# Optimization experiments

Hardware: AMD Instinct MI355X
Metric: run time of the kernel (lower is better)

The kernel has to match this reference:

```python
import jax, jax.numpy as jnp
import numpy as np

M, K, N, G = 64, 4096, 11008, 128  # tokens, infeatures, outfeatures, group_size
NUM_GROUPS = K // G  # 32


def _fp8_round_trip(w):
    # Simulate FP8 E4M3 storage of the quantized weight codes.
    return w.astype(jnp.float8_e4m3fn).astype(jnp.float32)


def setup_inputs() -> dict:
    key = jax.random.key(0)
    k1, k2, k3, k4 = jax.random.split(key, 4)
    x = jax.random.normal(k1, (M, K), dtype=jnp.float32)
    # FP8-representable weight codes (post round-trip, stored as f32 values)
    weight = _fp8_round_trip(jax.random.normal(k2, (N, K), dtype=jnp.float32) * 2.0)
    # Per-(out_feature, group) dequant scales, strictly positive
    weight_scale = jax.random.uniform(k3, (N, NUM_GROUPS), dtype=jnp.float32,
                                      minval=0.005, maxval=0.02)
    bias = jax.random.normal(k4, (N,), dtype=jnp.float32)
    return {"x": x, "weight": weight, "weight_scale": weight_scale, "bias": bias}


def reference(x, weight, weight_scale, bias):
    # Dequantize: each group of `G` consecutive in-features of an output row
    # shares one scale -> w_deq[o, i] = weight[o, i] * scale[o, i // G]
    n, k = weight.shape
    g = k // weight_scale.shape[1]
    w_deq = (weight.reshape(n, -1, g) * weight_scale[:, :, None]).reshape(n, k)
    # Fused dequant-matmul: out[m, o] = sum_i x[m, i] * w_deq[o, i] + bias[o]
    out = jnp.einsum("mk,nk->mn", x, w_deq) + bias
    return out
```

## Files before the change

kernel.cpp:

```cpp
#include <hip/hip_runtime.h>


#define Md 64
#define Kd 4096
#define Nd 11008
#define NGROUPS 32
#define BN 64
#define KSPLIT 16
#define KCHUNK (Kd / KSPLIT)
#define NSTEP (KCHUNK / 32)
#define NGRP (KCHUNK / 128)
#define KGS 64

typedef __attribute__((ext_vector_type(8))) __bf16 bf16x8;
typedef __attribute__((ext_vector_type(4))) float f32x4;

__global__ __launch_bounds__(256, 4)
void qlinear_pass1(const float* __restrict__ x,
                   const float* __restrict__ w,
                   const float* __restrict__ scale,
                   float* __restrict__ ws)
{
    const int tid  = threadIdx.x;
    const int wv   = tid >> 6;
    const int lane = tid & 63;
    const int quad = lane >> 4;
    const int ln   = lane & 15;

    const int n0 = blockIdx.x * BN;
    const int ky = blockIdx.y;
    const int k0 = ky * KCHUNK;

    __shared__ __bf16 lds_x[(KCHUNK / 8) * 64 * 8];

    {
        const int m = tid >> 2;
        const int q = tid & 3;
        const float* xp = x + (size_t)m * Kd + k0;
        #pragma unroll
        for (int j = 0; j < 4; ++j) {
            const int c = q * 16 + j * 64;
            float4 a = *(const float4*)(xp + c);
            float4 b = *(const float4*)(xp + c + 4);
            float4 e = *(const float4*)(xp + c + 8);
            float4 d = *(const float4*)(xp + c + 12);
            bf16x8 v0 = {(__bf16)a.x, (__bf16)a.y, (__bf16)a.z, (__bf16)a.w,
                         (__bf16)b.x, (__bf16)b.y, (__bf16)b.z, (__bf16)b.w};
            bf16x8 v1 = {(__bf16)e.x, (__bf16)e.y, (__bf16)e.z, (__bf16)e.w,
                         (__bf16)d.x, (__bf16)d.y, (__bf16)d.z, (__bf16)d.w};
            const int kg = c >> 3;
            *(bf16x8*)&lds_x[(size_t)(kg * KGS + m) * 8]       = v0;
            *(bf16x8*)&lds_x[(size_t)((kg + 1) * KGS + m) * 8] = v1;
        }
    }
    __syncthreads();

    const int nrow = n0 + wv * 16 + ln;
    const float* wp = w + (size_t)nrow * Kd + k0 + quad * 8;

    const float2 sc2 = *(const float2*)(scale + (size_t)nrow * NGROUPS
                                        + ky * NGRP);
    const float sc[2] = {sc2.x, sc2.y};

    f32x4 acc[4];
    #pragma unroll
    for (int t = 0; t < 4; ++t) acc[t] = (f32x4){0.f, 0.f, 0.f, 0.f};

    float4 wb[3][2];
    wb[0][0] = *(const float4*)(wp + 0);
    wb[0][1] = *(const float4*)(wp + 4);
    wb[1][0] = *(const float4*)(wp + 32);
    wb[1][1] = *(const float4*)(wp + 36);

    #pragma unroll
    for (int g = 0; g < NGRP; ++g) {
        f32x4 pg[4];
        #pragma unroll
        for (int t = 0; t < 4; ++t) pg[t] = (f32x4){0.f, 0.f, 0.f, 0.f};

        #pragma unroll
        for (int ks = 0; ks < 4; ++ks) {
            const int step = g * 4 + ks;
            if (step + 2 < NSTEP) {
                const int s = step + 2;
                wb[s % 3][0] = *(const float4*)(wp + s * 32);
                wb[s % 3][1] = *(const float4*)(wp + s * 32 + 4);
            }
            float4 wa = wb[step % 3][0], wbv = wb[step % 3][1];
            bf16x8 wf = {(__bf16)wa.x,  (__bf16)wa.y,  (__bf16)wa.z,  (__bf16)wa.w,
                         (__bf16)wbv.x, (__bf16)wbv.y, (__bf16)wbv.z, (__bf16)wbv.w};
            #pragma unroll
            for (int t = 0; t < 4; ++t) {
                bf16x8 xf = *(const bf16x8*)
                    &lds_x[(size_t)((step * 4 + quad) * KGS + t * 16 + ln) * 8];
                pg[t] = __builtin_amdgcn_mfma_f32_16x16x32_bf16(xf, wf, pg[t],
                                                                0, 0, 0);
            }
        }

        const float s = sc[g];
        #pragma unroll
        for (int t = 0; t < 4; ++t)
            #pragma unroll
            for (int r = 0; r < 4; ++r)
                acc[t][r] += s * pg[t][r];
    }

    float* op = ws + ((size_t)ky * Md) * Nd + n0 + wv * 16 + ln;
    #pragma unroll
    for (int t = 0; t < 4; ++t)
        #pragma unroll
        for (int r = 0; r < 4; ++r)
            op[(size_t)(t * 16 + quad * 4 + r) * Nd] = acc[t][r];
}

__global__ __launch_bounds__(256)
void qlinear_reduce(const float* __restrict__ ws,
                    const float* __restrict__ bias,
                    float* __restrict__ out)
{
    const int idx4 = blockIdx.x * 256 + threadIdx.x;
    if (idx4 >= Md * Nd / 4) return;
    const int n4 = idx4 % (Nd / 4);
    float4 v = *(const float4*)(bias + n4 * 4);
    #pragma unroll
    for (int ky = 0; ky < KSPLIT; ++ky) {
        float4 p = *(const float4*)(ws + (size_t)ky * Md * Nd + (size_t)idx4 * 4);
        v.x += p.x; v.y += p.y; v.z += p.z; v.w += p.w;
    }
    *(float4*)(out + (size_t)idx4 * 4) = v;
}

extern "C" void kernel_launch(void* const* d_in, const int* in_sizes, int n_in,
                              void* d_out, int out_size, void* d_ws, size_t ws_size,
                              hipStream_t stream) {
    const float* x     = (const float*)d_in[0];
    const float* w     = (const float*)d_in[1];
    const float* scale = (const float*)d_in[2];
    const float* bias  = (const float*)d_in[3];
    float* out = (float*)d_out;
    float* ws  = (float*)d_ws;

    dim3 grid1(Nd / BN, KSPLIT);
    qlinear_pass1<<<grid1, 256, 0, stream>>>(x, w, scale, ws);

    const int total4 = Md * Nd / 4;
    qlinear_reduce<<<(total4 + 255) / 256, 256, 0, stream>>>(ws, bias, out);
}
```

Baseline: 278.5 us.

## Pre-convert x to bf16 in a separate kernel and drop LDS staging

Adds a pre-pass kernel that converts x to bf16 once, in the MFMA-friendly interleaved layout, and stores it in the workspace. The main kernel then reads x fragments straight from global memory (L2-resident) with double buffering, removing the per-block LDS fill and __syncthreads. It also issues all weight loads for the chunk up front and folds the group scale into the weight before the bf16 conversion, so the separate per-group partial accumulators go away. The cost is an extra kernel launch, 16 more float4 registers per thread, and a slight change in rounding because the scale is applied before bf16 truncation.

After: 287.8 us. 1.03x slower.

```diff
diff --git a/kernel.cpp b/kernel.cpp
--- a/kernel.cpp
+++ b/kernel.cpp
@@ -7,16 +7,29 @@
 #define NGROUPS 32
 #define BN 64
 #define KSPLIT 16
-#define KCHUNK (Kd / KSPLIT)
-#define NSTEP (KCHUNK / 32)
-#define NGRP (KCHUNK / 128)
-#define KGS 64
+#define KCHUNK 256
+#define NSTEP 8
+#define WS_PART_BYTES ((size_t)KSPLIT * Md * Nd * 4)
 
 typedef __attribute__((ext_vector_type(8))) __bf16 bf16x8;
 typedef __attribute__((ext_vector_type(4))) float f32x4;
 
+__global__ __launch_bounds__(256)
+void xcvt_kernel(const float* __restrict__ x, __bf16* __restrict__ xbf)
+{
+    const int tid = blockIdx.x * 256 + threadIdx.x;
+    const int m   = tid >> 9;
+    const int kgg = tid & 511;
+    const float* xp = x + (size_t)m * Kd + kgg * 8;
+    float4 a = *(const float4*)xp;
+    float4 b = *(const float4*)(xp + 4);
+    bf16x8 v = {(__bf16)a.x, (__bf16)a.y, (__bf16)a.z, (__bf16)a.w,
+                (__bf16)b.x, (__bf16)b.y, (__bf16)b.z, (__bf16)b.w};
+    *(bf16x8*)(xbf + ((size_t)kgg * 64 + m) * 8) = v;
+}
+
 __global__ __launch_bounds__(256, 4)
-void qlinear_pass1(const float* __restrict__ x,
+void qlinear_pass1(const __bf16* __restrict__ xbf,
                    const float* __restrict__ w,
                    const float* __restrict__ scale,
                    float* __restrict__ ws)
@@ -29,81 +42,52 @@
 
     const int n0 = blockIdx.x * BN;
     const int ky = blockIdx.y;
-    const int k0 = ky * KCHUNK;
-
-    __shared__ __bf16 lds_x[(KCHUNK / 8) * 64 * 8];
-
-    {
-        const int m = tid >> 2;
-        const int q = tid & 3;
-        const float* xp = x + (size_t)m * Kd + k0;
-        #pragma unroll
-        for (int j = 0; j < 4; ++j) {
-            const int c = q * 16 + j * 64;
-            float4 a = *(const float4*)(xp + c);
-            float4 b = *(const float4*)(xp + c + 4);
-            float4 e = *(const float4*)(xp + c + 8);
-            float4 d = *(const float4*)(xp + c + 12);
-            bf16x8 v0 = {(__bf16)a.x, (__bf16)a.y, (__bf16)a.z, (__bf16)a.w,
-                         (__bf16)b.x, (__bf16)b.y, (__bf16)b.z, (__bf16)b.w};
-            bf16x8 v1 = {(__bf16)e.x, (__bf16)e.y, (__bf16)e.z, (__bf16)e.w,
-                         (__bf16)d.x, (__bf16)d.y, (__bf16)d.z, (__bf16)d.w};
-            const int kg = c >> 3;
-            *(bf16x8*)&lds_x[(size_t)(kg * KGS + m) * 8]       = v0;
-            *(bf16x8*)&lds_x[(size_t)((kg + 1) * KGS + m) * 8] = v1;
-        }
-    }
-    __syncthreads();
 
     const int nrow = n0 + wv * 16 + ln;
-    const float* wp = w + (size_t)nrow * Kd + k0 + quad * 8;
+    const float* wp = w + (size_t)nrow * Kd + ky * KCHUNK + quad * 8;
 
-    const float2 sc2 = *(const float2*)(scale + (size_t)nrow * NGROUPS
-                                        + ky * NGRP);
+    const float2 sc2 = *(const float2*)(scale + (size_t)nrow * NGROUPS + ky * 2);
     const float sc[2] = {sc2.x, sc2.y};
+
+    const __bf16* xb = xbf + ((size_t)ky * 32 * 64) * 8
+                     + ((size_t)quad * 64 + ln) * 8;
+
+    bf16x8 xq[2][4];
+    #pragma unroll
+    for (int t = 0; t < 4; ++t)
+        xq[0][t] = *(const bf16x8*)(xb + (size_t)t * 16 * 8);
+
+    float4 wreg[16];
+    #pragma unroll
+    for (int s = 0; s < NSTEP; ++s) {
+        wreg[2 * s]     = *(const float4*)(wp + s * 32);
+        wreg[2 * s + 1] = *(const float4*)(wp + s * 32 + 4);
+    }
 
     f32x4 acc[4];
     #pragma unroll
     for (int t = 0; t < 4; ++t) acc[t] = (f32x4){0.f, 0.f, 0.f, 0.f};
 
-    float4 wb[3][2];
-    wb[0][0] = *(const float4*)(wp + 0);
-    wb[0][1] = *(const float4*)(wp + 4);
-    wb[1][0] = *(const float4*)(wp + 32);
-    wb[1][1] = *(const float4*)(wp + 36);
+    #pragma unroll
+    for (int s = 0; s < NSTEP; ++s) {
+        if (s + 1 < NSTEP) {
+            const __bf16* xn = xb + (size_t)(s + 1) * 4 * 64 * 8;
+            #pragma unroll
+            for (int t = 0; t < 4; ++t)
+                xq[(s + 1) & 1][t] = *(const bf16x8*)(xn + (size_t)t * 16 * 8);
+        }
 
-    #pragma unroll
-    for (int g = 0; g < NGRP; ++g) {
-        f32x4 pg[4];
-        #pragma unroll
-        for (int t = 0; t < 4; ++t) pg[t] = (f32x4){0.f, 0.f, 0.f, 0.f};
+        const float ss = sc[s >> 2];
+        const float4 wa = wreg[2 * s], wb = wreg[2 * s + 1];
+        bf16x8 wf = {(__bf16)(wa.x * ss), (__bf16)(wa.y * ss),
+                     (__bf16)(wa.z * ss), (__bf16)(wa.w * ss),
+                     (__bf16)(wb.x * ss), (__bf16)(wb.y * ss),
+                     (__bf16)(wb.z * ss), (__bf16)(wb.w * ss)};
 
         #pragma unroll
-        for (int ks = 0; ks < 4; ++ks) {
-            const int step = g * 4 + ks;
-            if (step + 2 < NSTEP) {
-                const int s = step + 2;
-                wb[s % 3][0] = *(const float4*)(wp + s * 32);
-                wb[s % 3][1] = *(const float4*)(wp + s * 32 + 4);
-            }
-            float4 wa = wb[step % 3][0], wbv = wb[step % 3][1];
-            bf16x8 wf = {(__bf16)wa.x,  (__bf16)wa.y,  (__bf16)wa.z,  (__bf16)wa.w,
-                         (__bf16)wbv.x, (__bf16)wbv.y, (__bf16)wbv.z, (__bf16)wbv.w};
-            #pragma unroll
-            for (int t = 0; t < 4; ++t) {
-                bf16x8 xf = *(const bf16x8*)
-                    &lds_x[(size_t)((step * 4 + quad) * KGS + t * 16 + ln) * 8];
-                pg[t] = __builtin_amdgcn_mfma_f32_16x16x32_bf16(xf, wf, pg[t],
-                                                                0, 0, 0);
-            }
-        }
-
-        const float s = sc[g];
-        #pragma unroll
         for (int t = 0; t < 4; ++t)
-            #pragma unroll
-            for (int r = 0; r < 4; ++r)
-                acc[t][r] += s * pg[t][r];
+            acc[t] = __builtin_amdgcn_mfma_f32_16x16x32_bf16(xq[s & 1][t], wf,
+                                                             acc[t], 0, 0, 0);
     }
 
     float* op = ws + ((size_t)ky * Md) * Nd + n0 + wv * 16 + ln;
@@ -139,11 +123,15 @@
     const float* scale = (const float*)d_in[2];
     const float* bias  = (const float*)d_in[3];
     float* out = (float*)d_out;
-    float* ws  = (float*)d_ws;
+
+    float*  ws_part = (float*)d_ws;
+    __bf16* xbf     = (__bf16*)((char*)d_ws + WS_PART_BYTES);
+
+    xcvt_kernel<<<128, 256, 0, stream>>>(x, xbf);
 
     dim3 grid1(Nd / BN, KSPLIT);
-    qlinear_pass1<<<grid1, 256, 0, stream>>>(x, w, scale, ws);
+    qlinear_pass1<<<grid1, 256, 0, stream>>>(xbf, w, scale, ws_part);
 
     const int total4 = Md * Nd / 4;
-    qlinear_reduce<<<(total4 + 255) / 256, 256, 0, stream>>>(ws, bias, out);
+    qlinear_reduce<<<(total4 + 255) / 256, 256, 0, stream>>>(ws_part, bias, out);
 }
```
